# Performance work log

Hardware: AMD Instinct MI355X
Metric: run time of the kernel (lower is better)

## Reference

```python
import jax, jax.numpy as jnp
import numpy as np

H = 4           # attention heads
NEG_SLOPE = 0.2 # GATConv default leaky_relu slope
BN_EPS = 1e-5


def gat_conv(x, src, dst, W, a_src, a_dst, b, N):
    # PyG GATConv (concat=True, add_self_loops=True): self-loops appended by caller.
    C = W.shape[1] // H
    h = (x @ W).reshape(N, H, C)                      # [N,H,C]
    al_s = jnp.einsum('nhc,hc->nh', h, a_src)          # [N,H]
    al_d = jnp.einsum('nhc,hc->nh', h, a_dst)
    e = jax.nn.leaky_relu(al_s[src] + al_d[dst], NEG_SLOPE)   # [E,H]
    m = jax.ops.segment_max(e, dst, num_segments=N)            # per-dst softmax (stable)
    p = jnp.exp(e - m[dst])
    s = jax.ops.segment_sum(p, dst, num_segments=N)
    alpha = p / s[dst]                                          # [E,H]
    out = jax.ops.segment_sum(alpha[:, :, None] * h[src], dst, num_segments=N)  # [N,H,C]
    return out.reshape(N, H * C) + b


def mp_layer(x, src, dst, gw, gas, gad, gb, fw, fb, fg, fbeta, N):
    gat_out = gat_conv(x, src, dst, gw, gas, gad, gb, N)
    # feature_transform: Linear -> BatchNorm1d (eval: running_mean=0, running_var=1) -> ReLU
    y = x @ fw + fb
    y = y * (fg / jnp.sqrt(1.0 + BN_EPS)) + fbeta
    y = jax.nn.relu(y)
    return gat_out + y


def forward(x, edge_index, edge_attr, params):
    N = x.shape[0]
    loop = jnp.arange(N, dtype=edge_index.dtype)
    src = jnp.concatenate([edge_index[0], loop])   # add self loops (GATConv default)
    dst = jnp.concatenate([edge_index[1], loop])
    for p in params[:-1]:
        x = mp_layer(x, src, dst, *p, N)
        x = jax.nn.relu(x)   # dropout is identity in eval mode
    cw, cb = params[-1]
    return x @ cw + cb


def setup_inputs() -> dict:
    N, E, D, Hd, O = 80000, 1000000, 512, 128, 10
    key = jax.random.key(0)
    ks = jax.random.split(key, 40)
    ki = iter(range(40))

    def rn(shape, fan_in):
        return jax.random.normal(ks[next(ki)], shape, dtype=jnp.float32) / np.sqrt(fan_in)

    inp = {}
    inp['x'] = jax.random.normal(ks[next(ki)], (N, D), dtype=jnp.float32)
    inp['edge_index'] = jax.random.randint(ks[next(ki)], (2, E), 0, N, dtype=jnp.int64)
    inp['edge_attr'] = jax.random.uniform(ks[next(ki)], (E, 1), dtype=jnp.float32)
    dims = [D, Hd, Hd]
    for li, din in enumerate(dims):
        inp[f'l{li}_gw'] = rn((din, Hd), din)
        inp[f'l{li}_gas'] = rn((H, Hd // H), Hd // H)
        inp[f'l{li}_gad'] = rn((H, Hd // H), Hd // H)
        inp[f'l{li}_gb'] = jnp.zeros((Hd,), jnp.float32)
        inp[f'l{li}_fw'] = rn((din, Hd), din)
        inp[f'l{li}_fb'] = jnp.zeros((Hd,), jnp.float32)
        inp[f'l{li}_fg'] = jnp.ones((Hd,), jnp.float32)
        inp[f'l{li}_fbeta'] = jnp.zeros((Hd,), jnp.float32)
    inp['cls_w'] = rn((Hd, O), Hd)
    inp['cls_b'] = jnp.zeros((O,), jnp.float32)
    return inp


def reference(x, edge_index, edge_attr,
              l0_gw, l0_gas, l0_gad, l0_gb, l0_fw, l0_fb, l0_fg, l0_fbeta,
              l1_gw, l1_gas, l1_gad, l1_gb, l1_fw, l1_fb, l1_fg, l1_fbeta,
              l2_gw, l2_gas, l2_gad, l2_gb, l2_fw, l2_fb, l2_fg, l2_fbeta,
              cls_w, cls_b):
    params = [
        (l0_gw, l0_gas, l0_gad, l0_gb, l0_fw, l0_fb, l0_fg, l0_fbeta),
        (l1_gw, l1_gas, l1_gad, l1_gb, l1_fw, l1_fb, l1_fg, l1_fbeta),
        (l2_gw, l2_gas, l2_gad, l2_gb, l2_fw, l2_fb, l2_fg, l2_fbeta),
        (cls_w, cls_b),
    ]
    return forward(x, edge_index, edge_attr, params)
```

## Files before the change

kernel.cpp:

```cpp
#include <hip/hip_runtime.h>
#include <cstdint>
#include <cstddef>

#define HD 128
#define NEG_SLOPE 0.2f
#define BN_EPS 1e-5f

typedef __bf16 bf16x8 __attribute__((ext_vector_type(8)));
typedef float  f32x4  __attribute__((ext_vector_type(4)));

__device__ __forceinline__ unsigned short f2b(float f) {
    unsigned int u = __float_as_uint(f);
    u = (u + 0x7fffu + ((u >> 16) & 1u)) >> 16;
    return (unsigned short)u;
}
__device__ __forceinline__ unsigned int pack2(float lo, float hi) {
    return (unsigned int)f2b(lo) | ((unsigned int)f2b(hi) << 16);
}

__global__ void prep_w2(const float* __restrict__ gw, const float* __restrict__ fw,
                        unsigned short* __restrict__ Wt, int K)
{
    int t = blockIdx.x * 256 + threadIdx.x;
    if (t >= K * 256) return;
    int k = t >> 8, c = t & 255;
    float v = (c < 128) ? gw[(size_t)k * 128 + c] : fw[(size_t)k * 128 + (c - 128)];
    Wt[(size_t)c * K + k] = f2b(v);
}

__global__ __launch_bounds__(512, 4) void gemm_dual(
    const float* __restrict__ X, const unsigned short* __restrict__ Wt,
    unsigned short* __restrict__ hb, float* __restrict__ yb, int M, int K,
    const float* __restrict__ fb, const float* __restrict__ fg,
    const float* __restrict__ fbeta, const float* __restrict__ gb)
{
    __shared__ __align__(16) char smem[128 * 80 + 256 * 80];
    char* Asb = smem;
    char* Bsb = smem + 128 * 80;

    const int tid  = threadIdx.x;
    const int row0 = blockIdx.x * 128;
    const int w    = tid >> 6, lane = tid & 63;
    const int wm   = w & 1,  wn = w >> 1;
    const int m    = lane & 15, q = lane >> 4;

    const int ra = tid >> 2, ka = (tid & 3) * 8;
    const int rb = tid >> 1, kb = (tid & 1) * 16;

    int arow = row0 + ra; if (arow >= M) arow = M - 1;

    f32x4 acc[4][4];
#pragma unroll
    for (int rt = 0; rt < 4; rt++)
#pragma unroll
        for (int ct = 0; ct < 4; ct++) acc[rt][ct] = (f32x4){0.f, 0.f, 0.f, 0.f};

    const int aw = ra * 80 + ka * 2;
    const int bw = rb * 80 + kb * 2;

    float4 pa0, pa1;
    uint4  pb0, pb1;
    {
        const float* xr = X + (size_t)arow * K + ka;
        pa0 = *(const float4*)xr; pa1 = *(const float4*)(xr + 4);
        const unsigned short* wr = Wt + (size_t)rb * K + kb;
        pb0 = *(const uint4*)wr; pb1 = *(const uint4*)(wr + 8);
    }

    for (int ks = 0; ks < K; ks += 32) {
        __syncthreads();
        uint4 av;
        av.x = pack2(pa0.x, pa0.y); av.y = pack2(pa0.z, pa0.w);
        av.z = pack2(pa1.x, pa1.y); av.w = pack2(pa1.z, pa1.w);
        *(uint4*)(Asb + aw) = av;
        *(uint4*)(Bsb + bw)      = pb0;
        *(uint4*)(Bsb + bw + 16) = pb1;
        __syncthreads();

        int kn = ks + 32;
        if (kn < K) {
            const float* xr = X + (size_t)arow * K + kn + ka;
            pa0 = *(const float4*)xr; pa1 = *(const float4*)(xr + 4);
            const unsigned short* wr = Wt + (size_t)rb * K + kn + kb;
            pb0 = *(const uint4*)wr; pb1 = *(const uint4*)(wr + 8);
        }

        bf16x8 af[4], bfr[4];
#pragma unroll
        for (int rt = 0; rt < 4; rt++)
            af[rt] = *(const bf16x8*)(Asb + (64 * wm + rt * 16 + m) * 80 + q * 16);
#pragma unroll
        for (int ct = 0; ct < 4; ct++)
            bfr[ct] = *(const bf16x8*)(Bsb + (64 * wn + ct * 16 + m) * 80 + q * 16);
#pragma unroll
        for (int rt = 0; rt < 4; rt++)
#pragma unroll
            for (int ct = 0; ct < 4; ct++)
                acc[rt][ct] = __builtin_amdgcn_mfma_f32_16x16x32_bf16(af[rt], bfr[ct], acc[rt][ct], 0, 0, 0);
    }

    if (wn < 2) {
#pragma unroll
        for (int ct = 0; ct < 4; ct++) {
            int col = 64 * wn + ct * 16 + m;
#pragma unroll
            for (int rt = 0; rt < 4; rt++)
#pragma unroll
                for (int r = 0; r < 4; r++) {
                    int row = row0 + 64 * wm + rt * 16 + q * 4 + r;
                    if (row < M) hb[(size_t)row * HD + col] = f2b(acc[rt][ct][r]);
                }
        }
    } else {
        const float inv_bn = 1.0f / sqrtf(1.0f + BN_EPS);
#pragma unroll
        for (int ct = 0; ct < 4; ct++) {
            int col = 64 * (wn - 2) + ct * 16 + m;
            float g  = fg[col] * inv_bn;
            float bb = fb[col];
            float bt = fbeta[col];
            float gv = gb[col];
#pragma unroll
            for (int rt = 0; rt < 4; rt++)
#pragma unroll
                for (int r = 0; r < 4; r++) {
                    int row = row0 + 64 * wm + rt * 16 + q * 4 + r;
                    if (row < M) {
                        float y = (acc[rt][ct][r] + bb) * g + bt;
                        y = y > 0.f ? y : 0.f;
                        yb[(size_t)row * HD + col] = y + gv;
                    }
                }
        }
    }
}

__global__ void al_kernel(const unsigned short* __restrict__ h,
                          const float* __restrict__ a_src, const float* __restrict__ a_dst,
                          float* __restrict__ als, float* __restrict__ ald, int N)
{
    int t = blockIdx.x * blockDim.x + threadIdx.x;
    if (t >= N * 4) return;
    int n = t >> 2, hd = t & 3;
    const unsigned short* hp = h + (size_t)n * HD + hd * 32;
    const float* as = a_src + hd * 32;
    const float* ad = a_dst + hd * 32;
    float s1 = 0.f, s2 = 0.f;
#pragma unroll
    for (int i = 0; i < 32; i += 8) {
        uint4 hv = *(const uint4*)(hp + i);
        unsigned int u[4] = {hv.x, hv.y, hv.z, hv.w};
#pragma unroll
        for (int p = 0; p < 4; p++) {
            float f0 = __uint_as_float(u[p] << 16);
            float f1 = __uint_as_float(u[p] & 0xffff0000u);
            s1 += f0 * as[i + 2 * p] + f1 * as[i + 2 * p + 1];
            s2 += f0 * ad[i + 2 * p] + f1 * ad[i + 2 * p + 1];
        }
    }
    als[t] = s1; ald[t] = s2;
}

__global__ void hist_kernel(const int* __restrict__ ei, int E, int N, int* __restrict__ deg)
{
    int t = blockIdx.x * blockDim.x + threadIdx.x;
    if (t >= E + N) return;
    int d = (t < E) ? ei[E + t] : (t - E);
    atomicAdd(&deg[d], 1);
}

__global__ void scan1(const int* __restrict__ deg, int* __restrict__ rp,
                      int* __restrict__ bsum, int N)
{
    __shared__ int sh[256];
    int t = threadIdx.x;
    int i0 = blockIdx.x * 1024 + t * 4;
    int v[4];
#pragma unroll
    for (int j = 0; j < 4; j++) v[j] = (i0 + j < N) ? deg[i0 + j] : 0;
    int tot = v[0] + v[1] + v[2] + v[3];
    sh[t] = tot;
    __syncthreads();
    for (int off = 1; off < 256; off <<= 1) {
        int xv = (t >= off) ? sh[t - off] : 0;
        __syncthreads();
        sh[t] += xv;
        __syncthreads();
    }
    int run = sh[t] - tot;
    if (t == 255) bsum[blockIdx.x] = sh[255];
#pragma unroll
    for (int j = 0; j < 4; j++) {
        if (i0 + j < N) rp[i0 + j] = run;
        run += v[j];
    }
}

__global__ void scan2(int* __restrict__ bsum, int nb)
{
    if (threadIdx.x == 0 && blockIdx.x == 0) {
        int run = 0;
        for (int i = 0; i < nb; i++) { int v = bsum[i]; bsum[i] = run; run += v; }
    }
}

__global__ void scan3(int* __restrict__ rp, int* __restrict__ cur,
                      const int* __restrict__ bsum, int N, int Etot)
{
    int t = blockIdx.x * blockDim.x + threadIdx.x;
    if (t < N) {
        int v = rp[t] + bsum[t >> 10];
        rp[t] = v;
        cur[t] = v;
    } else if (t == N) {
        rp[N] = Etot;
    }
}

__global__ void scatter_kernel(const int* __restrict__ ei, int E, int N,
                               int* __restrict__ cur, int* __restrict__ col)
{
    int t = blockIdx.x * blockDim.x + threadIdx.x;
    if (t >= E + N) return;
    int s, d;
    if (t < E) { s = ei[t]; d = ei[E + t]; } else { s = t - E; d = t - E; }
    int p = atomicAdd(&cur[d], 1);
    col[p] = s;
}

__global__ __launch_bounds__(256) void agg_kernel(
    const unsigned short* __restrict__ h, const float* __restrict__ als,
    const float* __restrict__ ald, const int* __restrict__ rp,
    const int* __restrict__ col, float* __restrict__ xio, int N)
{
    int wid  = (blockIdx.x * blockDim.x + threadIdx.x) >> 6;
    int lane = threadIdx.x & 63;
    if (wid >= N) return;
    int beg = rp[wid], end = rp[wid + 1];

    int g = lane >> 4, c = lane & 15, hB = c >> 2;
    float ad_h = ald[wid * 4 + hB];
    float acc[8];
#pragma unroll
    for (int p = 0; p < 8; p++) acc[p] = 0.f;
    float wsum = 0.f;
    const unsigned short* hbase = h + c * 8;
    for (int j = beg + g; j < end; j += 4) {
        int s = col[j];
        float e = als[s * 4 + hB] + ad_h;
        e = e > 0.f ? e : NEG_SLOPE * e;
        float wgt = __expf(e);
        wsum += wgt;
        uint4 hv = *(const uint4*)(hbase + (size_t)s * HD);
        unsigned int uu[4] = {hv.x, hv.y, hv.z, hv.w};
#pragma unroll
        for (int p = 0; p < 4; p++) {
            acc[2 * p]     += wgt * __uint_as_float(uu[p] << 16);
            acc[2 * p + 1] += wgt * __uint_as_float(uu[p] & 0xffff0000u);
        }
    }
#pragma unroll
    for (int p = 0; p < 8; p++) {
        acc[p] += __shfl_xor(acc[p], 16);
        acc[p] += __shfl_xor(acc[p], 32);
    }
    wsum += __shfl_xor(wsum, 16);
    wsum += __shfl_xor(wsum, 32);
    if (g == 0) {
        float inv = 1.0f / wsum;
        float* xp = xio + (size_t)wid * HD + c * 8;
        float4 x0 = *(float4*)xp, x1 = *(float4*)(xp + 4);
        float o[8] = {acc[0] * inv + x0.x, acc[1] * inv + x0.y,
                      acc[2] * inv + x0.z, acc[3] * inv + x0.w,
                      acc[4] * inv + x1.x, acc[5] * inv + x1.y,
                      acc[6] * inv + x1.z, acc[7] * inv + x1.w};
#pragma unroll
        for (int p = 0; p < 8; p++) o[p] = o[p] > 0.f ? o[p] : 0.f;
        *(float4*)xp       = (float4){o[0], o[1], o[2], o[3]};
        *(float4*)(xp + 4) = (float4){o[4], o[5], o[6], o[7]};
    }
}

__global__ __launch_bounds__(256) void cls_kernel(
    const float* __restrict__ x, const float* __restrict__ w,
    const float* __restrict__ b, float* __restrict__ out, int N)
{
    int wid  = (blockIdx.x * blockDim.x + threadIdx.x) >> 6;
    int lane = threadIdx.x & 63;
    if (wid >= N) return;
    float x0 = x[(size_t)wid * HD + lane];
    float x1 = x[(size_t)wid * HD + 64 + lane];
    float acc[10];
#pragma unroll
    for (int o = 0; o < 10; o++)
        acc[o] = x0 * w[lane * 10 + o] + x1 * w[(lane + 64) * 10 + o];
#pragma unroll
    for (int o = 0; o < 10; o++) {
        float v = acc[o];
#pragma unroll
        for (int off = 1; off < 64; off <<= 1) v += __shfl_xor(v, off);
        acc[o] = v;
    }
    float v = 0.f;
#pragma unroll
    for (int o = 0; o < 10; o++) if (lane == o) v = acc[o];
    if (lane < 10) out[(size_t)wid * 10 + lane] = v + b[lane];
}

extern "C" void kernel_launch(void* const* d_in, const int* in_sizes, int n_in,
                              void* d_out, int out_size, void* d_ws, size_t ws_size,
                              hipStream_t stream)
{
    const float* x0 = (const float*)d_in[0];
    const int*   ei = (const int*)d_in[1];
    const int N = in_sizes[0] / 512;
    const int E = in_sizes[1] / 2;
    const int Etot = E + N;

    const float *gw[3], *gas[3], *gad[3], *gbp[3], *fw[3], *fbp[3], *fgp[3], *fbt[3];
    for (int l = 0; l < 3; l++) {
        int b = 3 + 8 * l;
        gw[l]  = (const float*)d_in[b + 0];
        gas[l] = (const float*)d_in[b + 1];
        gad[l] = (const float*)d_in[b + 2];
        gbp[l] = (const float*)d_in[b + 3];
        fw[l]  = (const float*)d_in[b + 4];
        fbp[l] = (const float*)d_in[b + 5];
        fgp[l] = (const float*)d_in[b + 6];
        fbt[l] = (const float*)d_in[b + 7];
    }
    const float* cw = (const float*)d_in[27];
    const float* cb = (const float*)d_in[28];

    char* p = (char*)d_ws;
    auto carve = [&](size_t bytes) -> char* {
        char* r = p; p += (bytes + 255) & ~(size_t)255; return r;
    };
    float* xA   = (float*)carve((size_t)N * HD * 4);
    float* xB   = (float*)carve((size_t)N * HD * 4);
    unsigned short* hbuf = (unsigned short*)carve((size_t)N * HD * 2);
    float* als  = (float*)carve((size_t)N * 4 * 4);
    float* ald  = (float*)carve((size_t)N * 4 * 4);
    int* rp   = (int*)carve((size_t)(N + 1) * 4);
    int* deg  = (int*)carve((size_t)N * 4);
    int* cur  = (int*)carve((size_t)N * 4);
    int* bsum = (int*)carve(4096);
    int* col  = (int*)carve((size_t)Etot * 4);
    unsigned short* wT[3];
    for (int l = 0; l < 3; l++) {
        int K = (l == 0) ? 512 : HD;
        wT[l] = (unsigned short*)carve((size_t)256 * K * 2);
    }

    for (int l = 0; l < 3; l++) {
        int K = (l == 0) ? 512 : HD;
        int nt = K * 256;
        prep_w2<<<(nt + 255) / 256, 256, 0, stream>>>(gw[l], fw[l], wT[l], K);
    }

    hipMemsetAsync(deg, 0, (size_t)N * 4, stream);
    hist_kernel<<<(Etot + 255) / 256, 256, 0, stream>>>(ei, E, N, deg);
    int nb = (N + 1023) / 1024;
    scan1<<<nb, 256, 0, stream>>>(deg, rp, bsum, N);
    scan2<<<1, 64, 0, stream>>>(bsum, nb);
    scan3<<<(N + 256) / 256, 256, 0, stream>>>(rp, cur, bsum, N, Etot);
    scatter_kernel<<<(Etot + 255) / 256, 256, 0, stream>>>(ei, E, N, cur, col);

    for (int l = 0; l < 3; l++) {
        const float* xin = (l == 0) ? x0 : ((l == 1) ? xA : xB);
        float* xout = (l == 1) ? xB : xA;
        int K = (l == 0) ? 512 : HD;
        int mblocks = (N + 127) / 128;
        gemm_dual<<<mblocks, 512, 0, stream>>>(xin, wT[l], hbuf, xout, N, K,
                                               fbp[l], fgp[l], fbt[l], gbp[l]);
        al_kernel<<<(N * 4 + 255) / 256, 256, 0, stream>>>(hbuf, gas[l], gad[l], als, ald, N);
        agg_kernel<<<(N + 3) / 4, 256, 0, stream>>>(hbuf, als, ald, rp, col, xout, N);
    }

    cls_kernel<<<(N + 3) / 4, 256, 0, stream>>>(xA, cw, cb, (float*)d_out, N);
}
```

Baseline: 782.2 us.

## Use direct global-to-LDS loads with swizzled layout in dual GEMM

The dual GEMM now loads X (fp32) and the transposed weights straight into LDS with global_load_lds, using XOR-swizzled layouts to avoid bank conflicts. The fp32-to-bf16 conversion moves to after the LDS read. The tile shrinks to 64 rows with 256 threads, each wave owning 64 output columns. This removes the register staging and VGPR pressure of the old path, but it also drops the register prefetch of the next K-slice, so loads are no longer overlapped with the MFMAs, and LDS traffic for A doubles because it is stored as fp32.

```diff
diff --git a/kernel.cpp b/kernel.cpp
--- a/kernel.cpp
+++ b/kernel.cpp
@@ -16,6 +16,12 @@
 }
 __device__ __forceinline__ unsigned int pack2(float lo, float hi) {
     return (unsigned int)f2b(lo) | ((unsigned int)f2b(hi) << 16);
+}
+
+__device__ __forceinline__ void gload_lds16(const void* g, void* l) {
+    __builtin_amdgcn_global_load_lds(
+        (const __attribute__((address_space(1))) uint32_t*)g,
+        (__attribute__((address_space(3))) uint32_t*)l, 16, 0, 0);
 }
 
 __global__ void prep_w2(const float* __restrict__ gw, const float* __restrict__ fw,
@@ -28,70 +34,75 @@
     Wt[(size_t)c * K + k] = f2b(v);
 }
 
-__global__ __launch_bounds__(512, 4) void gemm_dual(
+__global__ __launch_bounds__(256, 4) void gemm_dual(
     const float* __restrict__ X, const unsigned short* __restrict__ Wt,
     unsigned short* __restrict__ hb, float* __restrict__ yb, int M, int K,
     const float* __restrict__ fb, const float* __restrict__ fg,
     const float* __restrict__ fbeta, const float* __restrict__ gb)
 {
-    __shared__ __align__(16) char smem[128 * 80 + 256 * 80];
+    __shared__ __align__(16) char smem[64 * 128 + 256 * 64];
     char* Asb = smem;
-    char* Bsb = smem + 128 * 80;
+    char* Bsb = smem + 64 * 128;
 
     const int tid  = threadIdx.x;
-    const int row0 = blockIdx.x * 128;
-    const int w    = tid >> 6, lane = tid & 63;
-    const int wm   = w & 1,  wn = w >> 1;
-    const int m    = lane & 15, q = lane >> 4;
-
-    const int ra = tid >> 2, ka = (tid & 3) * 8;
-    const int rb = tid >> 1, kb = (tid & 1) * 16;
-
-    int arow = row0 + ra; if (arow >= M) arow = M - 1;
+    const int lane = tid & 63, w = tid >> 6;
+    const int row0 = blockIdx.x * 64;
+    const int m = lane & 15, q = lane >> 4;
+
+    const int la = lane >> 3, ca = lane & 7;
+    const int lb = lane >> 2, cb = lane & 3;
+    const int oA = 4 * (ca ^ la);
+    const int oB = 8 * (cb ^ (la & 3));
+
+    const float* ap[2];
+    const unsigned short* bp[4];
+#pragma unroll
+    for (int i = 0; i < 2; i++) {
+        int r  = (i * 4 + w) * 8 + la;
+        int gr = row0 + r; if (gr >= M) gr = M - 1;
+        ap[i] = X + (size_t)gr * K + oA;
+    }
+#pragma unroll
+    for (int i = 0; i < 4; i++) {
+        int r = (i * 4 + w) * 16 + lb;
+        bp[i] = Wt + (size_t)r * K + oB;
+    }
 
     f32x4 acc[4][4];
 #pragma unroll
     for (int rt = 0; rt < 4; rt++)
 #pragma unroll
         for (int ct = 0; ct < 4; ct++) acc[rt][ct] = (f32x4){0.f, 0.f, 0.f, 0.f};
-
-    const int aw = ra * 80 + ka * 2;
-    const int bw = rb * 80 + kb * 2;
-
-    float4 pa0, pa1;
-    uint4  pb0, pb1;
-    {
-        const float* xr = X + (size_t)arow * K + ka;
-        pa0 = *(const float4*)xr; pa1 = *(const float4*)(xr + 4);
-        const unsigned short* wr = Wt + (size_t)rb * K + kb;
-        pb0 = *(const uint4*)wr; pb1 = *(const uint4*)(wr + 8);
-    }
 
     for (int ks = 0; ks < K; ks += 32) {
         __syncthreads();
-        uint4 av;
-        av.x = pack2(pa0.x, pa0.y); av.y = pack2(pa0.z, pa0.w);
-        av.z = pack2(pa1.x, pa1.y); av.w = pack2(pa1.z, pa1.w);
-        *(uint4*)(Asb + aw) = av;
-        *(uint4*)(Bsb + bw)      = pb0;
-        *(uint4*)(Bsb + bw + 16) = pb1;
+#pragma unroll
+        for (int i = 0; i < 2; i++)
+            gload_lds16(ap[i] + ks, Asb + (i * 4 + w) * 1024);
+#pragma unroll
+        for (int i = 0; i < 4; i++)
+            gload_lds16(bp[i] + ks, Bsb + (i * 4 + w) * 1024);
         __syncthreads();
 
-        int kn = ks + 32;
-        if (kn < K) {
-            const float* xr = X + (size_t)arow * K + kn + ka;
-            pa0 = *(const float4*)xr; pa1 = *(const float4*)(xr + 4);
-            const unsigned short* wr = Wt + (size_t)rb * K + kn + kb;
-            pb0 = *(const uint4*)wr; pb1 = *(const uint4*)(wr + 8);
-        }
-
         bf16x8 af[4], bfr[4];
 #pragma unroll
-        for (int rt = 0; rt < 4; rt++)
-            af[rt] = *(const bf16x8*)(Asb + (64 * wm + rt * 16 + m) * 80 + q * 16);
-#pragma unroll
-        for (int ct = 0; ct < 4; ct++)
-            bfr[ct] = *(const bf16x8*)(Bsb + (64 * wn + ct * 16 + m) * 80 + q * 16);
+        for (int rt = 0; rt < 4; rt++) {
+            int row = rt * 16 + m;
+            const char* base = Asb + (row << 7);
+            int sw = (m & 7) << 4;
+            f32x4 a0 = *(const f32x4*)(base + ((q * 32)      ^ sw));
+            f32x4 a1 = *(const f32x4*)(base + ((q * 32 + 16) ^ sw));
+            uint4 av;
+            av.x = pack2(a0.x, a0.y); av.y = pack2(a0.z, a0.w);
+            av.z = pack2(a1.x, a1.y); av.w = pack2(a1.z, a1.w);
+            af[rt] = *(bf16x8*)&av;
+        }
+#pragma unroll
+        for (int ct = 0; ct < 4; ct++) {
+            int row = w * 64 + ct * 16 + m;
+            bfr[ct] = *(const bf16x8*)(Bsb + (row << 6) +
+                                       ((q * 16) ^ (((m >> 1) & 3) << 4)));
+        }
 #pragma unroll
         for (int rt = 0; rt < 4; rt++)
 #pragma unroll
@@ -99,15 +110,15 @@
                 acc[rt][ct] = __builtin_amdgcn_mfma_f32_16x16x32_bf16(af[rt], bfr[ct], acc[rt][ct], 0, 0, 0);
     }
 
-    if (wn < 2) {
+    if (w < 2) {
 #pragma unroll
         for (int ct = 0; ct < 4; ct++) {
-            int col = 64 * wn + ct * 16 + m;
+            int col = 64 * w + ct * 16 + m;
 #pragma unroll
             for (int rt = 0; rt < 4; rt++)
 #pragma unroll
                 for (int r = 0; r < 4; r++) {
-                    int row = row0 + 64 * wm + rt * 16 + q * 4 + r;
+                    int row = row0 + rt * 16 + q * 4 + r;
                     if (row < M) hb[(size_t)row * HD + col] = f2b(acc[rt][ct][r]);
                 }
         }
@@ -115,7 +126,7 @@
         const float inv_bn = 1.0f / sqrtf(1.0f + BN_EPS);
 #pragma unroll
         for (int ct = 0; ct < 4; ct++) {
-            int col = 64 * (wn - 2) + ct * 16 + m;
+            int col = 64 * (w - 2) + ct * 16 + m;
             float g  = fg[col] * inv_bn;
             float bb = fb[col];
             float bt = fbeta[col];
@@ -124,7 +135,7 @@
             for (int rt = 0; rt < 4; rt++)
 #pragma unroll
                 for (int r = 0; r < 4; r++) {
-                    int row = row0 + 64 * wm + rt * 16 + q * 4 + r;
+                    int row = row0 + rt * 16 + q * 4 + r;
                     if (row < M) {
                         float y = (acc[rt][ct][r] + bb) * g + bt;
                         y = y > 0.f ? y : 0.f;
@@ -370,8 +381,8 @@
         const float* xin = (l == 0) ? x0 : ((l == 1) ? xA : xB);
         float* xout = (l == 1) ? xB : xA;
         int K = (l == 0) ? 512 : HD;
-        int mblocks = (N + 127) / 128;
-        gemm_dual<<<mblocks, 512, 0, stream>>>(xin, wT[l], hbuf, xout, N, K,
+        int mblocks = (N + 63) / 64;
+        gemm_dual<<<mblocks, 256, 0, stream>>>(xin, wT[l], hbuf, xout, N, K,
                                                fbp[l], fgp[l], fbt[l], gbp[l]);
         al_kernel<<<(N * 4 + 255) / 256, 256, 0, stream>>>(hbuf, gas[l], gad[l], als, ald, N);
         agg_kernel<<<(N + 3) / 4, 256, 0, stream>>>(hbuf, als, ald, rp, col, xout, N);
```

New measurement: 791.2 us. No clear change (+1.2%).
